# Kernel tuning notes

Measured on AMD Instinct MI355X. Metric: run time of the kernel, lower is better.

## Reference

```python
import jax, jax.numpy as jnp
import numpy as np

N_NODES = 100000


def _mean_agg(x, src, dst, n_nodes):
    # mean of src-node features over in-edges of each dst node (DGL copy_u + mean)
    summed = jax.ops.segment_sum(x[src], dst, num_segments=n_nodes)  # [N, F]
    deg = jax.ops.segment_sum(jnp.ones_like(src, dtype=x.dtype), dst, num_segments=n_nodes)
    return summed / jnp.maximum(deg, 1.0)[:, None]  # nodes w/o in-edges -> 0


def _sage_conv(x, src, dst, W_self, W_neigh, b):
    # DGL SAGEConv('mean'): fc_self(h) + fc_neigh(mean_neigh(h)) + bias
    h_neigh = _mean_agg(x, src, dst, x.shape[0])
    return x @ W_self + h_neigh @ W_neigh + b


def setup_inputs() -> dict:
    key = jax.random.key(0)
    ks = jax.random.split(key, 8)
    F_IN, F_H, E = 128, 128, 1600000
    s = 1.0 / np.sqrt(F_IN)
    return {
        "x": jax.random.normal(ks[0], (N_NODES, F_IN), dtype=jnp.float32),
        "src": jax.random.randint(ks[1], (E,), 0, N_NODES, dtype=jnp.int64),
        "dst": jax.random.randint(ks[2], (E,), 0, N_NODES, dtype=jnp.int64),
        "W1_self": jax.random.normal(ks[3], (F_IN, F_H), dtype=jnp.float32) * s,
        "W1_neigh": jax.random.normal(ks[4], (F_IN, F_H), dtype=jnp.float32) * s,
        "b1": jnp.zeros((F_H,), dtype=jnp.float32),
        "W2_self": jax.random.normal(ks[5], (F_H, F_H), dtype=jnp.float32) * s,
        "W2_neigh": jax.random.normal(ks[6], (F_H, F_H), dtype=jnp.float32) * s,
        "b2": jnp.zeros((F_H,), dtype=jnp.float32),
    }


def reference(x, src, dst, W1_self, W1_neigh, b1, W2_self, W2_neigh, b2):
    h = _sage_conv(x, src, dst, W1_self, W1_neigh, b1)
    # dropout in eval mode == identity
    h = jax.nn.relu(h)
    return _sage_conv(h, src, dst, W2_self, W2_neigh, b2)
```

## Files before the change

### kernel.cpp

```cpp
#include <hip/hip_runtime.h>

#define F 128
#define NN 100000
#define NBUK 782
#define NBLK 256
#define LD 136
#define N4 (NN * F / 4)
#define SORT_CAP 8192

typedef __attribute__((ext_vector_type(8))) short short8;
typedef __attribute__((ext_vector_type(4))) float f32x4;
typedef __attribute__((ext_vector_type(2))) float f32x2;
typedef __attribute__((ext_vector_type(4))) int int4v;
typedef __attribute__((ext_vector_type(2))) int int2v;
typedef __attribute__((ext_vector_type(4))) unsigned short us4;
typedef unsigned short ushort_t;
typedef unsigned char uchar_t;

__device__ __forceinline__ ushort_t f2b(float f) {
    union { float f; unsigned u; } x;
    x.f = f;
    unsigned r = x.u + 0x7fffu + ((x.u >> 16) & 1u);
    return (ushort_t)(r >> 16);
}
__device__ __forceinline__ float b2f(ushort_t u) {
    union { unsigned u; float f; } x;
    x.u = ((unsigned)u) << 16;
    return x.f;
}

__device__ __forceinline__ unsigned f_to_e4m3(float v) {
    union { float f; unsigned b; } x; x.f = v;
    unsigned s = (x.b >> 24) & 0x80u;
    float a = fabsf(v);
    if (!(a < 448.f)) return s | 0x7Eu;
    if (a < 0.015625f) return s | (unsigned)__float2int_rn(a * 512.f);
    unsigned ab = x.b & 0x7FFFFFFFu;
    unsigned r = ab + 0x7FFFFu + ((ab >> 20) & 1u);
    unsigned e = (r >> 23) - 120u;
    return s | ((e << 3) | ((r >> 20) & 7u));
}
__device__ __forceinline__ float e4m3_to_f(unsigned u) {
    unsigned s = (u & 0x80u) << 24;
    unsigned e = (u >> 3) & 15u;
    unsigned m = u & 7u;
    union { unsigned b; float f; } x;
    x.b = s | ((e + 120u) << 23) | (m << 20);
    float f = x.f;
    if (e == 0) f = fmaf(f, 2.f, s ? 0.015625f : -0.015625f);
    return f;
}
__device__ __forceinline__ unsigned pack4_fp8(float f0, float f1, float f2, float f3) {
#if __has_builtin(__builtin_amdgcn_cvt_pk_fp8_f32)
    int w = 0;
    w = __builtin_amdgcn_cvt_pk_fp8_f32(f0, f1, w, false);
    w = __builtin_amdgcn_cvt_pk_fp8_f32(f2, f3, w, true);
    return (unsigned)w;
#else
    return f_to_e4m3(f0) | (f_to_e4m3(f1) << 8) | (f_to_e4m3(f2) << 16) |
           (f_to_e4m3(f3) << 24);
#endif
}
__device__ __forceinline__ void dec4(int w, float* o) {
#if __has_builtin(__builtin_amdgcn_cvt_pk_f32_fp8)
    f32x2 a = __builtin_amdgcn_cvt_pk_f32_fp8(w, false);
    f32x2 b = __builtin_amdgcn_cvt_pk_f32_fp8(w, true);
    o[0] = a[0]; o[1] = a[1]; o[2] = b[0]; o[3] = b[1];
#else
    o[0] = e4m3_to_f((unsigned)w & 0xFFu);
    o[1] = e4m3_to_f(((unsigned)w >> 8) & 0xFFu);
    o[2] = e4m3_to_f(((unsigned)w >> 16) & 0xFFu);
    o[3] = e4m3_to_f(((unsigned)w >> 24) & 0xFFu);
#endif
}

__device__ __forceinline__ int4v ld_row16(const ushort_t* p) {
    int4v r;
    asm volatile("global_load_dwordx4 %0, %1, off" : "=v"(r) : "v"(p) : "memory");
    return r;
}
__device__ __forceinline__ int2v ld_row8(const uchar_t* p) {
    int2v r;
    asm volatile("global_load_dwordx2 %0, %1, off" : "=v"(r) : "v"(p) : "memory");
    return r;
}

__global__ __launch_bounds__(256) void k1_fused(
    const int* __restrict__ dst, int* __restrict__ H, int E, int chunk,
    const float* __restrict__ Wa, const float* __restrict__ Wb,
    const float* __restrict__ Wc, const float* __restrict__ Wd,
    ushort_t* __restrict__ Oa, ushort_t* __restrict__ Ob,
    ushort_t* __restrict__ Oc, ushort_t* __restrict__ Od,
    const float* __restrict__ X, ushort_t* __restrict__ Y,
    uchar_t* __restrict__ X8) {
    __shared__ union {
        int h[NBUK];
        float tile[32][33];
    } u;
    const int blk = blockIdx.x;
    if (blk < NBLK) {
        for (int i = threadIdx.x; i < NBUK; i += 256) u.h[i] = 0;
        __syncthreads();
        const int s0 = blk * chunk, s1 = min(E, s0 + chunk);
        for (int i = s0 + threadIdx.x; i < s1; i += 256)
            atomicAdd(&u.h[dst[i] >> 7], 1);
        __syncthreads();
        for (int i = threadIdx.x; i < NBUK; i += 256)
            H[blk * NBUK + i] = u.h[i];
    } else if (blk < NBLK + 64) {
        const int m = (blk - NBLK) >> 4;
        const int b = (blk - NBLK) & 15;
        const float* W = (m == 0) ? Wa : (m == 1) ? Wb : (m == 2) ? Wc : Wd;
        ushort_t* WT = (m == 0) ? Oa : (m == 1) ? Ob : (m == 2) ? Oc : Od;
        const int by = (b >> 2) * 32;
        const int bx = (b & 3) * 32;
        const int tx = threadIdx.x & 31, ty = threadIdx.x >> 5;
        for (int i = 0; i < 32; i += 8)
            u.tile[ty + i][tx] = W[(by + ty + i) * F + bx + tx];
        __syncthreads();
        for (int i = 0; i < 32; i += 8)
            WT[(bx + ty + i) * F + by + tx] = f2b(u.tile[tx][ty + i]);
    } else {
        const int base = (blk - NBLK - 64) * 512;
#pragma unroll
        for (int k = 0; k < 2; k++) {
            const int i = base + k * 256 + threadIdx.x;
            if (i < N4) {
                float4 v = ((const float4*)X)[i];
                us4 o;
                o.x = f2b(v.x); o.y = f2b(v.y); o.z = f2b(v.z); o.w = f2b(v.w);
                ((us4*)Y)[i] = o;
                ((unsigned*)X8)[i] = pack4_fp8(v.x, v.y, v.z, v.w);
            }
        }
    }
}

__global__ __launch_bounds__(256) void scan_cols(int* __restrict__ H,
                                                 int* __restrict__ Htot) {
    __shared__ int s[NBLK];
    const int k = blockIdx.x;
    const int t = threadIdx.x;
    const int v = H[t * NBUK + k];
    s[t] = v;
    __syncthreads();
    for (int d = 1; d < NBLK; d <<= 1) {
        const int u = (t >= d) ? s[t - d] : 0;
        __syncthreads();
        s[t] += u;
        __syncthreads();
    }
    H[t * NBUK + k] = s[t] - v;
    if (t == NBLK - 1) Htot[k] = s[t];
}

__global__ __launch_bounds__(256) void scatter2(const int* __restrict__ src,
                                                const int* __restrict__ dst,
                                                const int* __restrict__ H,
                                                const int* __restrict__ Htot,
                                                int* __restrict__ boffs,
                                                unsigned* __restrict__ pairs,
                                                int E, int chunk) {
    __shared__ int cur[NBUK];
    __shared__ int part[256];
    const int b = blockIdx.x;
    const int t = threadIdx.x;
    int v0 = 0, v1 = 0, v2 = 0, v3 = 0;
    {
        const int base = t * 4;
        if (base + 0 < NBUK) v0 = Htot[base + 0];
        if (base + 1 < NBUK) v1 = Htot[base + 1];
        if (base + 2 < NBUK) v2 = Htot[base + 2];
        if (base + 3 < NBUK) v3 = Htot[base + 3];
    }
    const int own = v0 + v1 + v2 + v3;
    part[t] = own;
    __syncthreads();
    for (int d = 1; d < 256; d <<= 1) {
        const int u = (t >= d) ? part[t - d] : 0;
        __syncthreads();
        part[t] += u;
        __syncthreads();
    }
    {
        int run = part[t] - own;
        const int base = t * 4;
        if (base + 0 < NBUK) { cur[base + 0] = run + H[b * NBUK + base + 0]; if (b == 0) boffs[base + 0] = run; run += v0; }
        if (base + 1 < NBUK) { cur[base + 1] = run + H[b * NBUK + base + 1]; if (b == 0) boffs[base + 1] = run; run += v1; }
        if (base + 2 < NBUK) { cur[base + 2] = run + H[b * NBUK + base + 2]; if (b == 0) boffs[base + 2] = run; run += v2; }
        if (base + 3 < NBUK) { cur[base + 3] = run + H[b * NBUK + base + 3]; if (b == 0) boffs[base + 3] = run; run += v3; }
    }
    if (b == 0 && t == 0) boffs[NBUK] = E;
    __syncthreads();
    const int s0 = b * chunk, s1 = min(E, s0 + chunk);
    for (int i = s0 + t; i < s1; i += 256) {
        const int d = dst[i];
        const int p = atomicAdd(&cur[d >> 7], 1);
        pairs[p] = ((unsigned)(d & 127) << 20) | (unsigned)src[i];
    }
}

__global__ __launch_bounds__(256) void bucket_sort(const unsigned* __restrict__ pairs,
                                                   const int* __restrict__ boffs,
                                                   int* __restrict__ offs,
                                                   int* __restrict__ csr) {
    __shared__ int cnt[128], loffs[128], lcur[128];
    __shared__ unsigned sbuf[SORT_CAP];
    const int b = blockIdx.x, t = threadIdx.x;
    const int e0 = boffs[b], e1 = boffs[b + 1];
    const int n = e1 - e0;
    const int node0 = b << 7;
    const int nnode = min(128, NN - node0);
    if (t < 128) cnt[t] = 0;
    __syncthreads();
    for (int i = e0 + t; i < e1; i += 256) atomicAdd(&cnt[pairs[i] >> 20], 1);
    __syncthreads();
    if (t < 128) loffs[t] = cnt[t];
    __syncthreads();
    for (int d = 1; d < 128; d <<= 1) {
        int u = (t >= d && t < 128) ? loffs[t - d] : 0;
        __syncthreads();
        if (t < 128) loffs[t] += u;
        __syncthreads();
    }
    if (t < 128) {
        const int ex = loffs[t] - cnt[t];
        lcur[t] = ex;
        if (t < nnode) offs[node0 + t] = e0 + ex;
    }
    if (b == NBUK - 1 && t == 0) offs[NN] = e1;
    __syncthreads();

    if (n <= SORT_CAP) {
        for (int i = e0 + t; i < e1; i += 256) {
            const unsigned v = pairs[i];
            const int p = atomicAdd(&lcur[v >> 20], 1);
            sbuf[p] = v;
        }
        __syncthreads();
        for (int i = t; i < n; i += 256) {
            const unsigned v = sbuf[i];
            const int d = v >> 20;
            const int hi = loffs[d];
            const int lo = hi - cnt[d];
            int r = lo;
            for (int j = lo; j < hi; ++j) {
                const unsigned w = sbuf[j];
                r += (w < v) || (w == v && j < i);
            }
            csr[e0 + r] = (int)(v & 0xFFFFFu);
        }
    } else {
        for (int i = e0 + t; i < e1; i += 256) {
            const unsigned v = pairs[i];
            const int p = atomicAdd(&lcur[v >> 20], 1);
            csr[e0 + p] = (int)(v & 0xFFFFFu);
        }
    }
}

template <typename TOUT, int GF8>
__global__ __launch_bounds__(256) void sage_layer(
    const ushort_t* __restrict__ Xg, const uchar_t* __restrict__ X8g,
    const int* __restrict__ offs, const int* __restrict__ csr,
    const ushort_t* __restrict__ WTs, const ushort_t* __restrict__ WTn,
    const float* __restrict__ bias,
    TOUT* __restrict__ out, uchar_t* __restrict__ out8, int relu) {
    __shared__ __align__(16) ushort_t sX[32 * LD];
    __shared__ __align__(16) ushort_t sH[32 * LD];
    const int t = threadIdx.x;
    const int lane = t & 63;
    const int wave = t >> 6;
    const int brow0 = blockIdx.x * 32;

    {
        const ushort_t* base = Xg + (size_t)brow0 * F;
        for (int i = t; i < 32 * 16; i += 256) {
            int row = i >> 4, ch = i & 15;
            *(short8*)&sX[row * LD + ch * 8] = *(const short8*)&base[row * F + ch * 8];
        }
    }

    {
        const int slot = lane >> 4;
        const int cl = lane & 15;
        const int c8 = cl * 8;
#pragma unroll
        for (int rr = 0; rr < 2; rr++) {
            const int rloc = wave * 8 + slot * 2 + rr;
            const int row = brow0 + rloc;
            const int e0 = offs[row], e1 = offs[row + 1];
            const int d = e1 - e0;
            float acc[8];
#pragma unroll
            for (int j = 0; j < 8; j++) acc[j] = 0.f;
            if (d > 0) {
                const int e1m1 = e1 - 1;
                if constexpr (GF8) {
                    const int nb = (d + 15) >> 4;
#pragma unroll 1
                    for (int b = 0; b < nb; b++) {
                        const int e = e0 + b * 16;
#define IDX9(K) const int i##K = csr[min(e + K, e1m1)];
                        IDX9(0) IDX9(1) IDX9(2) IDX9(3) IDX9(4) IDX9(5) IDX9(6) IDX9(7)
                        IDX9(8) IDX9(9) IDX9(10) IDX9(11) IDX9(12) IDX9(13) IDX9(14) IDX9(15)
#undef IDX9
#define LDR9(K) int2v r##K = ld_row8(X8g + (size_t)i##K * F + c8);
                        LDR9(0) LDR9(1) LDR9(2) LDR9(3) LDR9(4) LDR9(5) LDR9(6) LDR9(7)
                        LDR9(8) LDR9(9) LDR9(10) LDR9(11) LDR9(12) LDR9(13) LDR9(14) LDR9(15)
#undef LDR9
                        asm volatile("s_waitcnt vmcnt(0)" ::: "memory");
                        asm volatile("" : "+v"(r0), "+v"(r1), "+v"(r2), "+v"(r3),
                                           "+v"(r4), "+v"(r5), "+v"(r6), "+v"(r7),
                                           "+v"(r8), "+v"(r9), "+v"(r10), "+v"(r11),
                                           "+v"(r12), "+v"(r13), "+v"(r14), "+v"(r15));
                        __builtin_amdgcn_sched_barrier(0);
#define ACC9(K) { float tv[8]; dec4(r##K.x, tv); dec4(r##K.y, tv + 4);            \
                  const float mk = (e + K < e1) ? 1.f : 0.f;                      \
                  _Pragma("unroll")                                               \
                  for (int j = 0; j < 8; j++) acc[j] = fmaf(mk, tv[j], acc[j]); }
                        ACC9(0) ACC9(1) ACC9(2) ACC9(3) ACC9(4) ACC9(5) ACC9(6) ACC9(7)
                        ACC9(8) ACC9(9) ACC9(10) ACC9(11) ACC9(12) ACC9(13) ACC9(14) ACC9(15)
#undef ACC9
                    }
                } else {
                    const int nb = (d + 7) >> 3;
#pragma unroll 1
                    for (int b = 0; b < nb; b++) {
                        const int e = e0 + b * 8;
                        const int i0 = csr[e];
                        const int i1 = csr[min(e + 1, e1m1)];
                        const int i2 = csr[min(e + 2, e1m1)];
                        const int i3 = csr[min(e + 3, e1m1)];
                        const int i4 = csr[min(e + 4, e1m1)];
                        const int i5 = csr[min(e + 5, e1m1)];
                        const int i6 = csr[min(e + 6, e1m1)];
                        const int i7 = csr[min(e + 7, e1m1)];
                        int4v r0 = ld_row16(Xg + (size_t)i0 * F + c8);
                        int4v r1 = ld_row16(Xg + (size_t)i1 * F + c8);
                        int4v r2 = ld_row16(Xg + (size_t)i2 * F + c8);
                        int4v r3 = ld_row16(Xg + (size_t)i3 * F + c8);
                        int4v r4 = ld_row16(Xg + (size_t)i4 * F + c8);
                        int4v r5 = ld_row16(Xg + (size_t)i5 * F + c8);
                        int4v r6 = ld_row16(Xg + (size_t)i6 * F + c8);
                        int4v r7 = ld_row16(Xg + (size_t)i7 * F + c8);
                        asm volatile("s_waitcnt vmcnt(0)" ::: "memory");
                        asm volatile("" : "+v"(r0), "+v"(r1), "+v"(r2), "+v"(r3),
                                           "+v"(r4), "+v"(r5), "+v"(r6), "+v"(r7));
                        __builtin_amdgcn_sched_barrier(0);
                        const short8 v0 = __builtin_bit_cast(short8, r0);
                        const short8 v1 = __builtin_bit_cast(short8, r1);
                        const short8 v2 = __builtin_bit_cast(short8, r2);
                        const short8 v3 = __builtin_bit_cast(short8, r3);
                        const short8 v4 = __builtin_bit_cast(short8, r4);
                        const short8 v5 = __builtin_bit_cast(short8, r5);
                        const short8 v6 = __builtin_bit_cast(short8, r6);
                        const short8 v7 = __builtin_bit_cast(short8, r7);
                        const float m1 = (e + 1 < e1) ? 1.f : 0.f;
                        const float m2 = (e + 2 < e1) ? 1.f : 0.f;
                        const float m3 = (e + 3 < e1) ? 1.f : 0.f;
                        const float m4 = (e + 4 < e1) ? 1.f : 0.f;
                        const float m5 = (e + 5 < e1) ? 1.f : 0.f;
                        const float m6 = (e + 6 < e1) ? 1.f : 0.f;
                        const float m7 = (e + 7 < e1) ? 1.f : 0.f;
#pragma unroll
                        for (int j = 0; j < 8; j++) {
                            float s01 = b2f((ushort_t)v0[j]) + m1 * b2f((ushort_t)v1[j]);
                            float s23 = m2 * b2f((ushort_t)v2[j]) + m3 * b2f((ushort_t)v3[j]);
                            float s45 = m4 * b2f((ushort_t)v4[j]) + m5 * b2f((ushort_t)v5[j]);
                            float s67 = m6 * b2f((ushort_t)v6[j]) + m7 * b2f((ushort_t)v7[j]);
                            acc[j] += (s01 + s23) + (s45 + s67);
                        }
                    }
                }
            }
            const float inv = (d > 0) ? (1.0f / (float)d) : 0.f;
            short8 o;
#pragma unroll
            for (int j = 0; j < 8; j++) o[j] = (short)f2b(acc[j] * inv);
            *(short8*)&sH[rloc * LD + c8] = o;
        }
    }
    __syncthreads();

    const int q = lane >> 4, nl = lane & 15;
    const int colbase = wave * 32;
    f32x4 acc00 = (f32x4)0.f, acc01 = (f32x4)0.f, acc10 = (f32x4)0.f, acc11 = (f32x4)0.f;
#pragma unroll
    for (int ks = 0; ks < 4; ks++) {
        const int ko = ks * 32 + q * 8;
        const short8 aS0 = *(const short8*)&sX[nl * LD + ko];
        const short8 aS1 = *(const short8*)&sX[(16 + nl) * LD + ko];
        const short8 aN0 = *(const short8*)&sH[nl * LD + ko];
        const short8 aN1 = *(const short8*)&sH[(16 + nl) * LD + ko];
        const size_t bo0 = (size_t)(colbase + nl) * F + ko;
        const size_t bo1 = (size_t)(colbase + 16 + nl) * F + ko;
        const short8 bS0 = *(const short8*)&WTs[bo0];
        const short8 bS1 = *(const short8*)&WTs[bo1];
        const short8 bN0 = *(const short8*)&WTn[bo0];
        const short8 bN1 = *(const short8*)&WTn[bo1];
        acc00 = __builtin_amdgcn_mfma_f32_16x16x32_bf16(aS0, bS0, acc00, 0, 0, 0);
        acc00 = __builtin_amdgcn_mfma_f32_16x16x32_bf16(aN0, bN0, acc00, 0, 0, 0);
        acc01 = __builtin_amdgcn_mfma_f32_16x16x32_bf16(aS0, bS1, acc01, 0, 0, 0);
        acc01 = __builtin_amdgcn_mfma_f32_16x16x32_bf16(aN0, bN1, acc01, 0, 0, 0);
        acc10 = __builtin_amdgcn_mfma_f32_16x16x32_bf16(aS1, bS0, acc10, 0, 0, 0);
        acc10 = __builtin_amdgcn_mfma_f32_16x16x32_bf16(aN1, bN0, acc10, 0, 0, 0);
        acc11 = __builtin_amdgcn_mfma_f32_16x16x32_bf16(aS1, bS1, acc11, 0, 0, 0);
        acc11 = __builtin_amdgcn_mfma_f32_16x16x32_bf16(aN1, bN1, acc11, 0, 0, 0);
    }

    const float b0 = bias[colbase + nl];
    const float b1 = bias[colbase + 16 + nl];
    if constexpr (sizeof(TOUT) == 2) {
        __syncthreads();
#pragma unroll
        for (int r = 0; r < 4; r++) {
            const int lr0 = q * 4 + r, lr1 = 16 + q * 4 + r;
            float v00 = acc00[r] + b0, v01 = acc01[r] + b1;
            float v10 = acc10[r] + b0, v11 = acc11[r] + b1;
            if (relu) {
                v00 = fmaxf(v00, 0.f); v01 = fmaxf(v01, 0.f);
                v10 = fmaxf(v10, 0.f); v11 = fmaxf(v11, 0.f);
            }
            sX[lr0 * LD + colbase + nl] = f2b(v00);
            sX[lr0 * LD + colbase + 16 + nl] = f2b(v01);
            sX[lr1 * LD + colbase + nl] = f2b(v10);
            sX[lr1 * LD + colbase + 16 + nl] = f2b(v11);
        }
        __syncthreads();
        TOUT* base = out + (size_t)brow0 * F;
        for (int i = t; i < 32 * 16; i += 256) {
            int row = i >> 4, ch = i & 15;
            const short8 v = *(const short8*)&sX[row * LD + ch * 8];
            *(short8*)&base[row * F + ch * 8] = v;
            if (out8) {
                float f[8];
#pragma unroll
                for (int j = 0; j < 8; j++) f[j] = b2f((ushort_t)v[j]);
                int2v p;
                p.x = (int)pack4_fp8(f[0], f[1], f[2], f[3]);
                p.y = (int)pack4_fp8(f[4], f[5], f[6], f[7]);
                *(int2v*)&out8[(size_t)(brow0 + row) * F + ch * 8] = p;
            }
        }
    } else {
#pragma unroll
        for (int r = 0; r < 4; r++) {
            const int orow0 = brow0 + q * 4 + r;
            const int orow1 = brow0 + 16 + q * 4 + r;
            float v00 = acc00[r] + b0, v01 = acc01[r] + b1;
            float v10 = acc10[r] + b0, v11 = acc11[r] + b1;
            if (relu) {
                v00 = fmaxf(v00, 0.f); v01 = fmaxf(v01, 0.f);
                v10 = fmaxf(v10, 0.f); v11 = fmaxf(v11, 0.f);
            }
            out[(size_t)orow0 * F + colbase + nl] = v00;
            out[(size_t)orow0 * F + colbase + 16 + nl] = v01;
            out[(size_t)orow1 * F + colbase + nl] = v10;
            out[(size_t)orow1 * F + colbase + 16 + nl] = v11;
        }
    }
}

extern "C" void kernel_launch(void* const* d_in, const int* in_sizes, int n_in,
                              void* d_out, int out_size, void* d_ws, size_t ws_size,
                              hipStream_t stream) {
    const float* x = (const float*)d_in[0];
    const int* src = (const int*)d_in[1];
    const int* dst = (const int*)d_in[2];
    const float* W1s = (const float*)d_in[3];
    const float* W1n = (const float*)d_in[4];
    const float* b1 = (const float*)d_in[5];
    const float* W2s = (const float*)d_in[6];
    const float* W2n = (const float*)d_in[7];
    const float* b2 = (const float*)d_in[8];
    float* out = (float*)d_out;

    const int E = in_sizes[1];
    const int N = NN;
    const int E4 = (E + 3) & ~3;
    const int chunk = (E + NBLK - 1) / NBLK;

    unsigned* pairs = (unsigned*)d_ws;
    int* csr = (int*)(pairs + E4);
    ushort_t* h1 = (ushort_t*)(csr + E4);
    ushort_t* WT1s = h1 + (size_t)N * F;
    ushort_t* WT1n = WT1s + F * F;
    ushort_t* WT2s = WT1n + F * F;
    ushort_t* WT2n = WT2s + F * F;
    int* offs = (int*)(WT2n + F * F);
    int* H = offs + (N + 1);
    int* boffs = H + NBLK * NBUK;
    int* Htot = boffs + (NBUK + 1);
    ushort_t* xb = (ushort_t*)d_out;
    uchar_t* x8 = (uchar_t*)d_out + (size_t)N * F * 2;
    size_t off8 = (size_t)((char*)(Htot + NBUK) - (char*)d_ws);
    off8 = (off8 + 7) & ~(size_t)7;
    uchar_t* h1f8 = (uchar_t*)d_ws + off8;
    const bool l2f8 = ws_size >= off8 + (size_t)N * F;

    const int cvt_blocks = (N4 + 511) / 512;
    k1_fused<<<NBLK + 64 + cvt_blocks, 256, 0, stream>>>(
        dst, H, E, chunk, W1s, W1n, W2s, W2n, WT1s, WT1n, WT2s, WT2n, x, xb, x8);
    scan_cols<<<NBUK, NBLK, 0, stream>>>(H, Htot);
    scatter2<<<NBLK, 256, 0, stream>>>(src, dst, H, Htot, boffs, pairs, E, chunk);
    bucket_sort<<<NBUK, 256, 0, stream>>>(pairs, boffs, offs, csr);

    sage_layer<ushort_t, 1><<<N / 32, 256, 0, stream>>>(
        xb, x8, offs, csr, WT1s, WT1n, b1, h1, l2f8 ? h1f8 : nullptr, 1);
    if (l2f8) {
        sage_layer<float, 1><<<N / 32, 256, 0, stream>>>(
            h1, h1f8, offs, csr, WT2s, WT2n, b2, out, nullptr, 0);
    } else {
        sage_layer<float, 0><<<N / 32, 256, 0, stream>>>(
            h1, nullptr, offs, csr, WT2s, WT2n, b2, out, nullptr, 0);
    }
}
```

Baseline: 332.6 us.

## Replace bucketed two-level CSR sort with global-atomic degree count and direct scatter

The CSR build no longer uses per-block bucket histograms, a column scan, a bucketed pair scatter and an in-bucket sort. It now counts per-node degrees with global atomics, runs a two-kernel prefix scan over node degrees, and scatters src indices straight into the CSR with per-node atomic cursors. This removes the intermediate pairs buffer and the bucket_sort pass. In exchange it relies on contended global atomics and writes edges in nondeterministic order within each node, which changes floating-point summation order.

```diff
diff --git a/kernel.cpp b/kernel.cpp
--- a/kernel.cpp
+++ b/kernel.cpp
@@ -2,11 +2,10 @@
 
 #define F 128
 #define NN 100000
-#define NBUK 782
-#define NBLK 256
+#define NB2 ((NN + 1023) / 1024)
+#define HBLK 256
 #define LD 136
 #define N4 (NN * F / 4)
-#define SORT_CAP 8192
 
 typedef __attribute__((ext_vector_type(8))) short short8;
 typedef __attribute__((ext_vector_type(4))) float f32x4;
@@ -86,42 +85,34 @@
 }
 
 __global__ __launch_bounds__(256) void k1_fused(
-    const int* __restrict__ dst, int* __restrict__ H, int E, int chunk,
+    const int* __restrict__ dst, int* __restrict__ deg, int E,
     const float* __restrict__ Wa, const float* __restrict__ Wb,
     const float* __restrict__ Wc, const float* __restrict__ Wd,
     ushort_t* __restrict__ Oa, ushort_t* __restrict__ Ob,
     ushort_t* __restrict__ Oc, ushort_t* __restrict__ Od,
     const float* __restrict__ X, ushort_t* __restrict__ Y,
     uchar_t* __restrict__ X8) {
-    __shared__ union {
-        int h[NBUK];
-        float tile[32][33];
-    } u;
+    __shared__ float tile[32][33];
     const int blk = blockIdx.x;
-    if (blk < NBLK) {
-        for (int i = threadIdx.x; i < NBUK; i += 256) u.h[i] = 0;
-        __syncthreads();
-        const int s0 = blk * chunk, s1 = min(E, s0 + chunk);
-        for (int i = s0 + threadIdx.x; i < s1; i += 256)
-            atomicAdd(&u.h[dst[i] >> 7], 1);
-        __syncthreads();
-        for (int i = threadIdx.x; i < NBUK; i += 256)
-            H[blk * NBUK + i] = u.h[i];
-    } else if (blk < NBLK + 64) {
-        const int m = (blk - NBLK) >> 4;
-        const int b = (blk - NBLK) & 15;
+    if (blk < HBLK) {
+        const int stride = HBLK * 256;
+        for (int i = blk * 256 + threadIdx.x; i < E; i += stride)
+            atomicAdd(&deg[dst[i]], 1);
+    } else if (blk < HBLK + 64) {
+        const int m = (blk - HBLK) >> 4;
+        const int b = (blk - HBLK) & 15;
         const float* W = (m == 0) ? Wa : (m == 1) ? Wb : (m == 2) ? Wc : Wd;
         ushort_t* WT = (m == 0) ? Oa : (m == 1) ? Ob : (m == 2) ? Oc : Od;
         const int by = (b >> 2) * 32;
         const int bx = (b & 3) * 32;
         const int tx = threadIdx.x & 31, ty = threadIdx.x >> 5;
         for (int i = 0; i < 32; i += 8)
-            u.tile[ty + i][tx] = W[(by + ty + i) * F + bx + tx];
+            tile[ty + i][tx] = W[(by + ty + i) * F + bx + tx];
         __syncthreads();
         for (int i = 0; i < 32; i += 8)
-            WT[(bx + ty + i) * F + by + tx] = f2b(u.tile[tx][ty + i]);
+            WT[(bx + ty + i) * F + by + tx] = f2b(tile[tx][ty + i]);
     } else {
-        const int base = (blk - NBLK - 64) * 512;
+        const int base = (blk - HBLK - 64) * 512;
 #pragma unroll
         for (int k = 0; k < 2; k++) {
             const int i = base + k * 256 + threadIdx.x;
@@ -136,126 +127,63 @@
     }
 }
 
-__global__ __launch_bounds__(256) void scan_cols(int* __restrict__ H,
-                                                 int* __restrict__ Htot) {
-    __shared__ int s[NBLK];
-    const int k = blockIdx.x;
+__global__ __launch_bounds__(1024) void block_sums(const int* __restrict__ deg,
+                                                   int* __restrict__ bsum) {
+    __shared__ int s[1024];
     const int t = threadIdx.x;
-    const int v = H[t * NBUK + k];
+    const int gid = blockIdx.x * 1024 + t;
+    s[t] = (gid < NN) ? deg[gid] : 0;
+    __syncthreads();
+    for (int d = 512; d > 0; d >>= 1) {
+        if (t < d) s[t] += s[t + d];
+        __syncthreads();
+    }
+    if (t == 0) bsum[blockIdx.x] = s[0];
+}
+
+__global__ __launch_bounds__(1024) void scan_write(const int* __restrict__ deg,
+                                                   const int* __restrict__ bsum,
+                                                   int* __restrict__ offs,
+                                                   int* __restrict__ gcur, int E) {
+    __shared__ int sb[128];
+    __shared__ int s[1024];
+    const int t = threadIdx.x, b = blockIdx.x;
+    if (t < 128) sb[t] = (t < NB2) ? bsum[t] : 0;
+    __syncthreads();
+    for (int d = 1; d < 128; d <<= 1) {
+        const int u = (t >= d && t < 128) ? sb[t - d] : 0;
+        __syncthreads();
+        if (t < 128) sb[t] += u;
+        __syncthreads();
+    }
+    const int pb = (b == 0) ? 0 : sb[b - 1];
+    const int gid = b * 1024 + t;
+    const int v = (gid < NN) ? deg[gid] : 0;
     s[t] = v;
     __syncthreads();
-    for (int d = 1; d < NBLK; d <<= 1) {
+    for (int d = 1; d < 1024; d <<= 1) {
         const int u = (t >= d) ? s[t - d] : 0;
         __syncthreads();
         s[t] += u;
         __syncthreads();
     }
-    H[t * NBUK + k] = s[t] - v;
-    if (t == NBLK - 1) Htot[k] = s[t];
-}
-
-__global__ __launch_bounds__(256) void scatter2(const int* __restrict__ src,
-                                                const int* __restrict__ dst,
-                                                const int* __restrict__ H,
-                                                const int* __restrict__ Htot,
-                                                int* __restrict__ boffs,
-                                                unsigned* __restrict__ pairs,
-                                                int E, int chunk) {
-    __shared__ int cur[NBUK];
-    __shared__ int part[256];
-    const int b = blockIdx.x;
-    const int t = threadIdx.x;
-    int v0 = 0, v1 = 0, v2 = 0, v3 = 0;
-    {
-        const int base = t * 4;
-        if (base + 0 < NBUK) v0 = Htot[base + 0];
-        if (base + 1 < NBUK) v1 = Htot[base + 1];
-        if (base + 2 < NBUK) v2 = Htot[base + 2];
-        if (base + 3 < NBUK) v3 = Htot[base + 3];
-    }
-    const int own = v0 + v1 + v2 + v3;
-    part[t] = own;
-    __syncthreads();
-    for (int d = 1; d < 256; d <<= 1) {
-        const int u = (t >= d) ? part[t - d] : 0;
-        __syncthreads();
-        part[t] += u;
-        __syncthreads();
-    }
-    {
-        int run = part[t] - own;
-        const int base = t * 4;
-        if (base + 0 < NBUK) { cur[base + 0] = run + H[b * NBUK + base + 0]; if (b == 0) boffs[base + 0] = run; run += v0; }
-        if (base + 1 < NBUK) { cur[base + 1] = run + H[b * NBUK + base + 1]; if (b == 0) boffs[base + 1] = run; run += v1; }
-        if (base + 2 < NBUK) { cur[base + 2] = run + H[b * NBUK + base + 2]; if (b == 0) boffs[base + 2] = run; run += v2; }
-        if (base + 3 < NBUK) { cur[base + 3] = run + H[b * NBUK + base + 3]; if (b == 0) boffs[base + 3] = run; run += v3; }
-    }
-    if (b == 0 && t == 0) boffs[NBUK] = E;
-    __syncthreads();
-    const int s0 = b * chunk, s1 = min(E, s0 + chunk);
-    for (int i = s0 + t; i < s1; i += 256) {
+    const int off = pb + s[t] - v;
+    if (gid < NN) {
+        offs[gid] = off;
+        gcur[gid] = off;
+    }
+    if (gid == NN) offs[NN] = E;
+}
+
+__global__ __launch_bounds__(256) void scatter_direct(const int* __restrict__ src,
+                                                      const int* __restrict__ dst,
+                                                      int* __restrict__ gcur,
+                                                      int* __restrict__ csr, int E) {
+    const int stride = HBLK * 256;
+    for (int i = blockIdx.x * 256 + threadIdx.x; i < E; i += stride) {
         const int d = dst[i];
-        const int p = atomicAdd(&cur[d >> 7], 1);
-        pairs[p] = ((unsigned)(d & 127) << 20) | (unsigned)src[i];
-    }
-}
-
-__global__ __launch_bounds__(256) void bucket_sort(const unsigned* __restrict__ pairs,
-                                                   const int* __restrict__ boffs,
-                                                   int* __restrict__ offs,
-                                                   int* __restrict__ csr) {
-    __shared__ int cnt[128], loffs[128], lcur[128];
-    __shared__ unsigned sbuf[SORT_CAP];
-    const int b = blockIdx.x, t = threadIdx.x;
-    const int e0 = boffs[b], e1 = boffs[b + 1];
-    const int n = e1 - e0;
-    const int node0 = b << 7;
-    const int nnode = min(128, NN - node0);
-    if (t < 128) cnt[t] = 0;
-    __syncthreads();
-    for (int i = e0 + t; i < e1; i += 256) atomicAdd(&cnt[pairs[i] >> 20], 1);
-    __syncthreads();
-    if (t < 128) loffs[t] = cnt[t];
-    __syncthreads();
-    for (int d = 1; d < 128; d <<= 1) {
-        int u = (t >= d && t < 128) ? loffs[t - d] : 0;
-        __syncthreads();
-        if (t < 128) loffs[t] += u;
-        __syncthreads();
-    }
-    if (t < 128) {
-        const int ex = loffs[t] - cnt[t];
-        lcur[t] = ex;
-        if (t < nnode) offs[node0 + t] = e0 + ex;
-    }
-    if (b == NBUK - 1 && t == 0) offs[NN] = e1;
-    __syncthreads();
-
-    if (n <= SORT_CAP) {
-        for (int i = e0 + t; i < e1; i += 256) {
-            const unsigned v = pairs[i];
-            const int p = atomicAdd(&lcur[v >> 20], 1);
-            sbuf[p] = v;
-        }
-        __syncthreads();
-        for (int i = t; i < n; i += 256) {
-            const unsigned v = sbuf[i];
-            const int d = v >> 20;
-            const int hi = loffs[d];
-            const int lo = hi - cnt[d];
-            int r = lo;
-            for (int j = lo; j < hi; ++j) {
-                const unsigned w = sbuf[j];
-                r += (w < v) || (w == v && j < i);
-            }
-            csr[e0 + r] = (int)(v & 0xFFFFFu);
-        }
-    } else {
-        for (int i = e0 + t; i < e1; i += 256) {
-            const unsigned v = pairs[i];
-            const int p = atomicAdd(&lcur[v >> 20], 1);
-            csr[e0 + p] = (int)(v & 0xFFFFFu);
-        }
+        const int p = atomicAdd(&gcur[d], 1);
+        csr[p] = src[i];
     }
 }
 
@@ -479,32 +407,31 @@
     const int E = in_sizes[1];
     const int N = NN;
     const int E4 = (E + 3) & ~3;
-    const int chunk = (E + NBLK - 1) / NBLK;
-
-    unsigned* pairs = (unsigned*)d_ws;
-    int* csr = (int*)(pairs + E4);
+
+    int* csr = (int*)d_ws;
     ushort_t* h1 = (ushort_t*)(csr + E4);
     ushort_t* WT1s = h1 + (size_t)N * F;
     ushort_t* WT1n = WT1s + F * F;
     ushort_t* WT2s = WT1n + F * F;
     ushort_t* WT2n = WT2s + F * F;
     int* offs = (int*)(WT2n + F * F);
-    int* H = offs + (N + 1);
-    int* boffs = H + NBLK * NBUK;
-    int* Htot = boffs + (NBUK + 1);
+    int* deg = offs + (N + 1);
+    int* gcur = deg + N;
+    int* bsum = gcur + N;
     ushort_t* xb = (ushort_t*)d_out;
     uchar_t* x8 = (uchar_t*)d_out + (size_t)N * F * 2;
-    size_t off8 = (size_t)((char*)(Htot + NBUK) - (char*)d_ws);
+    size_t off8 = (size_t)((char*)(bsum + 128) - (char*)d_ws);
     off8 = (off8 + 7) & ~(size_t)7;
     uchar_t* h1f8 = (uchar_t*)d_ws + off8;
     const bool l2f8 = ws_size >= off8 + (size_t)N * F;
 
+    hipMemsetAsync(deg, 0, (size_t)N * sizeof(int), stream);
     const int cvt_blocks = (N4 + 511) / 512;
-    k1_fused<<<NBLK + 64 + cvt_blocks, 256, 0, stream>>>(
-        dst, H, E, chunk, W1s, W1n, W2s, W2n, WT1s, WT1n, WT2s, WT2n, x, xb, x8);
-    scan_cols<<<NBUK, NBLK, 0, stream>>>(H, Htot);
-    scatter2<<<NBLK, 256, 0, stream>>>(src, dst, H, Htot, boffs, pairs, E, chunk);
-    bucket_sort<<<NBUK, 256, 0, stream>>>(pairs, boffs, offs, csr);
+    k1_fused<<<HBLK + 64 + cvt_blocks, 256, 0, stream>>>(
+        dst, deg, E, W1s, W1n, W2s, W2n, WT1s, WT1n, WT2s, WT2n, x, xb, x8);
+    block_sums<<<NB2, 1024, 0, stream>>>(deg, bsum);
+    scan_write<<<NB2, 1024, 0, stream>>>(deg, bsum, offs, gcur, E);
+    scatter_direct<<<HBLK, 256, 0, stream>>>(src, dst, gcur, csr, E);
 
     sage_layer<ushort_t, 1><<<N / 32, 256, 0, stream>>>(
         xb, x8, offs, csr, WT1s, WT1n, b1, h1, l2f8 ? h1f8 : nullptr, 1);
```

After: 414.1 us. 24.5% more time.
